# Optimization experiments

Hardware: AMD Instinct MI355X
Metric: run time of the kernel (lower is better)

Reference implementation:

```python
import jax, jax.numpy as jnp
import numpy as np

DIM = 256
CTX_DIM = 256
HEADS = 32
DIM_HEAD = 32
INNER = HEADS * DIM_HEAD


def mish(x):
    return x * jnp.tanh(jax.nn.softplus(x))


def setup_inputs() -> dict:
    key = jax.random.key(0)
    ks = jax.random.split(key, 16)
    B, Lq, Lp = 16, 128, 512
    s = 0.02
    return {
        "x": jax.random.normal(ks[0], (B * Lq, DIM), jnp.float32),
        "context": jax.random.normal(ks[1], (B * Lp, CTX_DIM), jnp.float32),
        "batch_dis": jax.random.normal(ks[2], (B, Lp, Lq, 3), jnp.float32),
        "batch_dis_emb": jax.random.normal(ks[3], (B, Lp, Lq, HEADS), jnp.float32),
        "protein_len": Lp,
        "ligand_len": Lq,
        # params ([in, out] layout, torch Linear transposed)
        "W_qk": jax.random.normal(ks[4], (DIM, INNER), jnp.float32) * s,
        "W_v": jax.random.normal(ks[5], (DIM, INNER), jnp.float32) * s,
        "W_cqk": jax.random.normal(ks[6], (CTX_DIM, INNER), jnp.float32) * s,
        "W_cv": jax.random.normal(ks[7], (CTX_DIM, INNER), jnp.float32) * s,
        "W_m1": jax.random.normal(ks[8], (2 * HEADS, 4 * HEADS), jnp.float32) * s,
        "W_m2": jax.random.normal(ks[9], (4 * HEADS, 2 * HEADS), jnp.float32) * s,
        "b_m2": jnp.zeros((2 * HEADS,), jnp.float32),
        "W_o": jax.random.normal(ks[10], (INNER, DIM), jnp.float32) * s,
        "b_o": jnp.zeros((DIM,), jnp.float32),
        "W_d1": jax.random.normal(ks[11], (HEADS, 2 * HEADS), jnp.float32) * s,
        "b_d1": jnp.zeros((2 * HEADS,), jnp.float32),
        "W_d2": jax.random.normal(ks[12], (2 * HEADS, HEADS), jnp.float32) * s,
        "b_d2": jnp.zeros((HEADS,), jnp.float32),
    }


def reference(x, context, batch_dis, batch_dis_emb, protein_len, ligand_len,
              W_qk, W_v, W_cqk, W_cv, W_m1, W_m2, b_m2, W_o, b_o,
              W_d1, b_d1, W_d2, b_d2):
    h, dh = HEADS, DIM_HEAD
    scale = dh ** -0.5
    B = x.shape[0] // ligand_len
    # projections; split heads: [B, L, h, dh]
    qk = (x @ W_qk).reshape(B, ligand_len, h, dh)
    cqk = (context @ W_cqk).reshape(B, protein_len, h, dh)
    cv = (context @ W_cv).reshape(B, protein_len, h, dh)
    # ligand->protein attention scores: [B, h, Lq, Lp]
    sim = jnp.einsum('bihd,bjhd->bhij', qk, cqk) * scale
    # distance-embedding channels: [B, Lp, Lq, h] -> [B, h, Lq, Lp]
    dis = jnp.transpose(batch_dis_emb, (0, 3, 2, 1))
    s = jnp.concatenate([sim, dis], axis=1)           # [B, 2h, Lq, Lp]
    s = jnp.moveaxis(s, 1, -1)                        # [B, Lq, Lp, 2h]
    s = mish(s @ W_m1) @ W_m2 + b_m2                  # attn_mlp over channel dim
    attn = jax.nn.softmax(s, axis=2)                  # softmax over protein (j)
    # first h heads attend into context values
    out = jnp.einsum('bijh,bjhd->bihd', attn[..., :h], cv)
    out = out.reshape(B * ligand_len, h * dh) @ W_o + b_o   # [N_lig, dim]
    # last h heads aggregate 3D distance vectors
    out_dis = jnp.einsum('bijh,bjid->bidh', attn[..., h:], batch_dis)
    out_dis = out_dis.reshape(B * ligand_len, 3, h)
    out_dis = mish(out_dis @ W_d1 + b_d1) @ W_d2 + b_d2      # [N_lig, 3, h]
    return out, out_dis
```

## Files before the change

### kernel.cpp

```cpp
#include <hip/hip_runtime.h>

typedef unsigned short u16;
typedef unsigned int   u32;
typedef __attribute__((ext_vector_type(8))) short bf16x8;
typedef __attribute__((ext_vector_type(4))) float f32x4;

#define MFMA_BF16 __builtin_amdgcn_mfma_f32_16x16x32_bf16
#define LOG2E 1.4426950408889634f

__device__ __forceinline__ u16 f2bf(float f) {
    u32 x = __builtin_bit_cast(u32, f);
    u32 r = (x + 0x7fffu + ((x >> 16) & 1u)) >> 16;
    return (u16)r;
}
__device__ __forceinline__ u32 cvt_pk_bf16(float lo, float hi) {
    u32 r;
    asm("v_cvt_pk_bf16_f32 %0, %1, %2" : "=v"(r) : "v"(lo), "v"(hi));
    return r;
}
__device__ __forceinline__ float exp2_asm(float x) {
    float r;
    asm("v_exp_f32 %0, %1" : "=v"(r) : "v"(x));
    return r;
}
__device__ __forceinline__ float rcp_asm(float x) {
    float r;
    asm("v_rcp_f32 %0, %1" : "=v"(r) : "v"(x));
    return r;
}
__device__ __forceinline__ float mishf(float x) {
    float e = exp2_asm(x * LOG2E);
    float p = 1.f + e;
    float d = __builtin_fmaf(p, p, 1.f);
    float r = __builtin_fmaf(-2.f, rcp_asm(d), 1.f);
    return x * r;
}

__global__ __launch_bounds__(256) void gemm_mfma(
    const float* __restrict__ A, const float* __restrict__ W, u16* __restrict__ C,
    int M, int N, int K, float scale)
{
    __shared__ u16 As[128 * 40];
    __shared__ u16 Bf[4 * 64 * 8];

    const int tid = threadIdx.x;
    const int lane = tid & 63, wv = tid >> 6;
    const int qd = lane >> 4, ln = lane & 15;
    const int m0 = blockIdx.y * 128, n0 = blockIdx.x * 64;

    f32x4 acc[2][4];
#pragma unroll
    for (int a = 0; a < 2; ++a)
#pragma unroll
        for (int nt = 0; nt < 4; ++nt) acc[a][nt] = (f32x4){0.f, 0.f, 0.f, 0.f};

    for (int k0 = 0; k0 < K; k0 += 32) {
        {
            int r = tid >> 1, kh = (tid & 1) * 16;
            const float* ap = A + (size_t)(m0 + r) * K + k0 + kh;
            float4 a0 = ((const float4*)ap)[0];
            float4 a1 = ((const float4*)ap)[1];
            float4 a2 = ((const float4*)ap)[2];
            float4 a3 = ((const float4*)ap)[3];
            uint4 p0, p1;
            p0.x = cvt_pk_bf16(a0.x, a0.y);
            p0.y = cvt_pk_bf16(a0.z, a0.w);
            p0.z = cvt_pk_bf16(a1.x, a1.y);
            p0.w = cvt_pk_bf16(a1.z, a1.w);
            p1.x = cvt_pk_bf16(a2.x, a2.y);
            p1.y = cvt_pk_bf16(a2.z, a2.w);
            p1.z = cvt_pk_bf16(a3.x, a3.y);
            p1.w = cvt_pk_bf16(a3.z, a3.w);
            *(uint4*)&As[r * 40 + kh]     = p0;
            *(uint4*)&As[r * 40 + kh + 8] = p1;
        }
        {
            int nt = tid >> 6, q = (tid >> 4) & 3, nn = tid & 15;
            const float* wp = W + (size_t)(k0 + q * 8) * N + n0 + nt * 16 + nn;
            float w0 = wp[0], w1 = wp[(size_t)1 * N], w2 = wp[(size_t)2 * N], w3 = wp[(size_t)3 * N];
            float w4 = wp[(size_t)4 * N], w5 = wp[(size_t)5 * N], w6 = wp[(size_t)6 * N], w7 = wp[(size_t)7 * N];
            uint4 u;
            u.x = cvt_pk_bf16(w0, w1);
            u.y = cvt_pk_bf16(w2, w3);
            u.z = cvt_pk_bf16(w4, w5);
            u.w = cvt_pk_bf16(w6, w7);
            *(uint4*)&Bf[tid * 8] = u;
        }
        __syncthreads();
        bf16x8 af0 = *(const bf16x8*)&As[(wv * 32 + ln) * 40 + qd * 8];
        bf16x8 af1 = *(const bf16x8*)&As[(wv * 32 + 16 + ln) * 40 + qd * 8];
#pragma unroll
        for (int nt = 0; nt < 4; ++nt) {
            bf16x8 bfr = *(const bf16x8*)&Bf[(nt * 64 + lane) * 8];
            acc[0][nt] = MFMA_BF16(af0, bfr, acc[0][nt], 0, 0, 0);
            acc[1][nt] = MFMA_BF16(af1, bfr, acc[1][nt], 0, 0, 0);
        }
        __syncthreads();
    }
#pragma unroll
    for (int a = 0; a < 2; ++a)
#pragma unroll
        for (int nt = 0; nt < 4; ++nt) {
            u32 pk0 = cvt_pk_bf16(acc[a][nt][0] * scale, acc[a][nt][1] * scale);
            u32 pk1 = cvt_pk_bf16(acc[a][nt][2] * scale, acc[a][nt][3] * scale);
            size_t base = (size_t)(m0 + wv * 32 + a * 16 + qd * 4) * N + n0 + nt * 16 + ln;
            C[base]               = (u16)pk0;
            C[base + (size_t)N]   = (u16)(pk0 >> 16);
            C[base + (size_t)2*N] = (u16)pk1;
            C[base + (size_t)3*N] = (u16)(pk1 >> 16);
        }
}

__global__ __launch_bounds__(256) void transpose_cv(
    const u16* __restrict__ cv, u16* __restrict__ cvT)
{
    __shared__ u16 T[64 * 80];
    const int tid = threadIdx.x;
    const int ct = blockIdx.x * 64, jt = blockIdx.y * 64, b = blockIdx.z;
    {
        int j_l = tid >> 2, seg = tid & 3;
        const u16* src = cv + (size_t)(b * 512 + jt + j_l) * 1024 + ct + seg * 16;
        uint4 v0 = ((const uint4*)src)[0];
        uint4 v1 = ((const uint4*)src)[1];
        u16* tp = &T[seg * 16 * 80 + j_l];
        tp[0*80] = (u16)(v0.x & 0xffff); tp[1*80] = (u16)(v0.x >> 16);
        tp[2*80] = (u16)(v0.y & 0xffff); tp[3*80] = (u16)(v0.y >> 16);
        tp[4*80] = (u16)(v0.z & 0xffff); tp[5*80] = (u16)(v0.z >> 16);
        tp[6*80] = (u16)(v0.w & 0xffff); tp[7*80] = (u16)(v0.w >> 16);
        tp[8*80] = (u16)(v1.x & 0xffff); tp[9*80] = (u16)(v1.x >> 16);
        tp[10*80] = (u16)(v1.y & 0xffff); tp[11*80] = (u16)(v1.y >> 16);
        tp[12*80] = (u16)(v1.z & 0xffff); tp[13*80] = (u16)(v1.z >> 16);
        tp[14*80] = (u16)(v1.w & 0xffff); tp[15*80] = (u16)(v1.w >> 16);
    }
    __syncthreads();
    {
        int ch_l = tid >> 2, sg = tid & 3;
        u16* dst = cvT + (size_t)(b * 1024 + ct + ch_l) * 512 + jt + sg * 16;
        ((uint4*)dst)[0] = *(const uint4*)&T[ch_l * 80 + sg * 16];
        ((uint4*)dst)[1] = *(const uint4*)&T[ch_l * 80 + sg * 16 + 8];
    }
}

__global__ __launch_bounds__(256) void prep(
    const float* __restrict__ Wo, const float* __restrict__ W1, const float* __restrict__ W2,
    u16* __restrict__ WoT, u16* __restrict__ w1b, u16* __restrict__ w2b)
{
    const int bb = blockIdx.x, t = threadIdx.x;
    if (bb < 256) {
#pragma unroll
        for (int kk = 0; kk < 4; ++kk)
            WoT[(size_t)t * 1024 + bb * 4 + kk] = f2bf(Wo[(size_t)(bb * 4 + kk) * 256 + t]);
    } else {
        for (int u = 0; u < 32; ++u) {
            int idx = t + 256 * u;
            int j = idx & 7, lane = (idx >> 3) & 63, f = idx >> 9;
            int n = lane & 15, q = lane >> 4, ntc = f & 7, ks = f >> 3;
            w1b[idx] = f2bf(W1[(ks * 32 + q * 8 + j) * 128 + ntc * 16 + n]);
        }
        for (int u = 0; u < 32; ++u) {
            int idx = t + 256 * u;
            int j = idx & 7, lane = (idx >> 3) & 63, f = idx >> 9;
            int n = lane & 15, q = lane >> 4, ot = f & 3, ks = f >> 2;
            int k = q * 8 + j;
            int ch = ((k & 1) << 4) | (k >> 1);
            w2b[idx] = f2bf(W2[(ks * 32 + ch) * 64 + ot * 16 + n] * LOG2E);
        }
    }
}

__global__ __launch_bounds__(256, 1) void attn5(
    const u16* __restrict__ qk,
    const u16* __restrict__ cqk,
    const u16* __restrict__ cvT,
    const float* __restrict__ bde,
    const float* __restrict__ bdis,
    const u16* __restrict__ w1b, const u16* __restrict__ w2b,
    const float* __restrict__ b2,
    float* __restrict__ partial)
{
    __shared__ __align__(16) char smem[62976];
    u16*   ES  = (u16*)smem;
    u16*   MT  = (u16*)(smem + 20480);
    float* BD  = (float*)(smem + 25600);
    u16*   EST = (u16*)(smem + 29696);
    u16*   W1B = (u16*)(smem + 54784);

    const int tid = threadIdx.x;
    const int lane = tid & 63, wv = tid >> 6;
    const int qd = lane >> 4, ln = lane & 15;
    const int nblk = blockIdx.x;
    const int xcd = nblk & 7, g = nblk >> 3;
    const int b = xcd * 2 + (g & 1);
    const int r2 = g >> 1;
    const int it = r2 >> 2, jq = r2 & 3;
    const int i0 = it * 16;
    const int pidx = (b * 8 + it) * 4 + jq;

    for (int k = tid; k < 4096; k += 256) ((u32*)W1B)[k] = ((const u32*)w1b)[k];

    float b2r[4];
#pragma unroll
    for (int ot = 0; ot < 4; ++ot) b2r[ot] = b2[ot * 16 + ln] * LOG2E;

    bf16x8 qkf[8];
#pragma unroll
    for (int hh = 0; hh < 8; ++hh) {
        int h = wv * 8 + hh;
        qkf[hh] = *(const bf16x8*)(qk + ((size_t)(b * 128 + i0 + ln)) * 1024 + h * 32 + qd * 8);
    }

    f32x4 oacc[8][2];
#pragma unroll
    for (int a = 0; a < 8; ++a)
#pragma unroll
        for (int c = 0; c < 2; ++c) oacc[a][c] = (f32x4){0.f, 0.f, 0.f, 0.f};
    float dn[4][4] = {};
    float dd[4][3][2] = {};

    __syncthreads();

#pragma clang loop unroll(disable)
    for (int ps = 0; ps < 8; ++ps) {
        const int jg0 = jq * 128 + ps * 16;

        {
            const u16* crow = cqk + (size_t)(b * 512 + jg0 + ln) * 1024 + qd * 8;
#pragma unroll
            for (int hh = 0; hh < 4; ++hh) {
                const int h0 = wv * 8 + hh * 2;
                bf16x8 b0 = *(const bf16x8*)(crow + h0 * 32);
                bf16x8 b1 = *(const bf16x8*)(crow + (h0 + 1) * 32);
                f32x4 c0 = (f32x4){0.f, 0.f, 0.f, 0.f}, c1 = c0;
                c0 = MFMA_BF16(qkf[hh * 2],     b0, c0, 0, 0, 0);
                c1 = MFMA_BF16(qkf[hh * 2 + 1], b1, c1, 0, 0, 0);
#pragma unroll
                for (int r = 0; r < 4; ++r)
                    *(u32*)&ES[((qd * 4 + r) * 16 + ln) * 40 + h0] = cvt_pk_bf16(c0[r], c1[r]);
            }
        }
        {
            int ii = tid & 15, jj = tid >> 4;
            const float* sp = bdis + ((size_t)(b * 512 + jg0 + jj) * 128 + i0 + ii) * 3;
            float4 v4;
            v4.x = sp[0]; v4.y = sp[1]; v4.z = sp[2]; v4.w = 0.f;
            *(float4*)&BD[(ii * 16 + jj) * 4] = v4;
        }
        __syncthreads();

#pragma unroll
        for (int s = 0; s < 4; ++s) {
            const int i_loc = wv * 4 + s;
            bf16x8 af0 = *(const bf16x8*)&ES[(i_loc * 16 + ln) * 40 + qd * 8];
            bf16x8 af1;
            {
                const float* dp = bde + (((size_t)(b * 512 + jg0 + ln)) * 128 + i0 + i_loc) * 32 + qd * 8;
                float4 a0 = ((const float4*)dp)[0];
                float4 a1 = ((const float4*)dp)[1];
                uint4 u;
                u.x = cvt_pk_bf16(a0.x, a0.y);
                u.y = cvt_pk_bf16(a0.z, a0.w);
                u.z = cvt_pk_bf16(a1.x, a1.y);
                u.w = cvt_pk_bf16(a1.z, a1.w);
                af1 = __builtin_bit_cast(bf16x8, u);
            }
            f32x4 uacc[4];
#pragma unroll
            for (int ot = 0; ot < 4; ++ot) uacc[ot] = (f32x4){0.f, 0.f, 0.f, 0.f};
            u16* mt = MT + wv * 640;
#pragma unroll
            for (int cg = 0; cg < 4; ++cg) {
                bf16x8 w00 = *(const bf16x8*)&W1B[((cg * 2 + 0) * 64 + lane) * 8];
                bf16x8 w01 = *(const bf16x8*)&W1B[((cg * 2 + 1) * 64 + lane) * 8];
                bf16x8 w10 = *(const bf16x8*)&W1B[((8 + cg * 2 + 0) * 64 + lane) * 8];
                bf16x8 w11 = *(const bf16x8*)&W1B[((8 + cg * 2 + 1) * 64 + lane) * 8];
                f32x4 t0 = (f32x4){0.f, 0.f, 0.f, 0.f}, t1 = t0;
                t0 = MFMA_BF16(af0, w00, t0, 0, 0, 0);
                t0 = MFMA_BF16(af1, w10, t0, 0, 0, 0);
                t1 = MFMA_BF16(af0, w01, t1, 0, 0, 0);
                t1 = MFMA_BF16(af1, w11, t1, 0, 0, 0);
#pragma unroll
                for (int r = 0; r < 4; ++r) {
                    u32 pk = cvt_pk_bf16(mishf(t0[r]), mishf(t1[r]));
                    *(u32*)&mt[(qd * 4 + r) * 40 + (ln << 1)] = pk;
                }
                bf16x8 ta = *(const bf16x8*)&mt[ln * 40 + qd * 8];
#pragma unroll
                for (int ot = 0; ot < 4; ++ot) {
                    bf16x8 wf = *(const bf16x8*)(w2b + ((size_t)(cg * 4 + ot) * 64 + lane) * 8);
                    uacc[ot] = MFMA_BF16(ta, wf, uacc[ot], 0, 0, 0);
                }
            }
            float Ev[4][4];
#pragma unroll
            for (int ot = 0; ot < 4; ++ot) {
#pragma unroll
                for (int r = 0; r < 4; ++r) Ev[ot][r] = exp2_asm(uacc[ot][r] + b2r[ot]);
                dn[s][ot] += (Ev[ot][0] + Ev[ot][1]) + (Ev[ot][2] + Ev[ot][3]);
            }
#pragma unroll
            for (int r = 0; r < 4; ++r) {
                float4 bp = *(const float4*)&BD[(i_loc * 16 + qd * 4 + r) * 4];
                dd[s][0][0] += Ev[2][r] * bp.x; dd[s][0][1] += Ev[3][r] * bp.x;
                dd[s][1][0] += Ev[2][r] * bp.y; dd[s][1][1] += Ev[3][r] * bp.y;
                dd[s][2][0] += Ev[2][r] * bp.z; dd[s][2][1] += Ev[3][r] * bp.z;
            }
#pragma unroll
            for (int ot = 0; ot < 2; ++ot) {
                const int base = (ot * 16 + ln) * 392 + i_loc * 24 + qd * 4;
                *(u32*)&EST[base]     = cvt_pk_bf16(Ev[ot][0], Ev[ot][1]);
                *(u32*)&EST[base + 2] = cvt_pk_bf16(Ev[ot][2], Ev[ot][3]);
            }
        }
        __syncthreads();

#pragma unroll
        for (int hh = 0; hh < 8; ++hh) {
            const int h = wv * 8 + hh;
            bf16x8 af = (bf16x8){0, 0, 0, 0, 0, 0, 0, 0};
            if (qd < 2) af = *(const bf16x8*)&EST[h * 392 + ln * 24 + qd * 8];
#pragma unroll
            for (int nt = 0; nt < 2; ++nt) {
                bf16x8 bfr = (bf16x8){0, 0, 0, 0, 0, 0, 0, 0};
                if (qd < 2)
                    bfr = *(const bf16x8*)(cvT + ((size_t)(b * 1024 + h * 32 + nt * 16 + ln)) * 512 + jg0 + qd * 8);
                oacc[hh][nt] = MFMA_BF16(af, bfr, oacc[hh][nt], 0, 0, 0);
            }
        }
        __syncthreads();
    }

    float* P = partial + (size_t)pidx * 18944;
#pragma unroll
    for (int hh = 0; hh < 8; ++hh)
#pragma unroll
        for (int nt = 0; nt < 2; ++nt)
#pragma unroll
            for (int r = 0; r < 4; ++r)
                P[(size_t)(qd * 4 + r) * 1024 + (wv * 8 + hh) * 32 + nt * 16 + ln] = oacc[hh][nt][r];
#pragma unroll
    for (int s = 0; s < 4; ++s)
#pragma unroll
        for (int ot = 0; ot < 4; ++ot) {
            float v = dn[s][ot];
            v += __shfl_xor(v, 16, 64);
            v += __shfl_xor(v, 32, 64);
            if (qd == 0) P[16384 + (wv * 4 + s) * 64 + ot * 16 + ln] = v;
        }
#pragma unroll
    for (int s = 0; s < 4; ++s)
#pragma unroll
        for (int d = 0; d < 3; ++d)
#pragma unroll
            for (int o = 0; o < 2; ++o) {
                float v = dd[s][d][o];
                v += __shfl_xor(v, 16, 64);
                v += __shfl_xor(v, 32, 64);
                if (qd == 0) P[17408 + (wv * 4 + s) * 96 + d * 32 + o * 16 + ln] = v;
            }
}

__global__ __launch_bounds__(256, 2) void finalize(
    const float* __restrict__ partial, const u16* __restrict__ WoT,
    const float* __restrict__ bo,
    const float* __restrict__ Wd1, const float* __restrict__ bd1,
    const float* __restrict__ Wd2, const float* __restrict__ bd2,
    float* __restrict__ out0, float* __restrict__ out1)
{
    __shared__ float denomL[1024];
    __shared__ u16 preL[16 * 1032];
    __shared__ float odisL[1536];
    __shared__ float r1L[3072];

    const int tid = threadIdx.x;
    const int f = blockIdx.x;
    const int b = f >> 3, it = f & 7;
    const int row0 = b * 128 + it * 16;
    const float* P0 = partial + (size_t)(f * 4 + 0) * 18944;
    const float* P1 = partial + (size_t)(f * 4 + 1) * 18944;
    const float* P2 = partial + (size_t)(f * 4 + 2) * 18944;
    const float* P3 = partial + (size_t)(f * 4 + 3) * 18944;

    for (int k = tid; k < 1024; k += 256)
        denomL[k] = P0[16384 + k] + P1[16384 + k] + P2[16384 + k] + P3[16384 + k];
    __syncthreads();

    {
        const int h = tid >> 3;
#pragma unroll
        for (int i = 0; i < 16; ++i) {
            float4 a = *(const float4*)&P0[(size_t)i * 1024 + tid * 4];
            float4 bq = *(const float4*)&P1[(size_t)i * 1024 + tid * 4];
            float4 c = *(const float4*)&P2[(size_t)i * 1024 + tid * 4];
            float4 d = *(const float4*)&P3[(size_t)i * 1024 + tid * 4];
            float rdn = 1.f / denomL[i * 64 + h];
            u32 p0 = cvt_pk_bf16((a.x + bq.x + c.x + d.x) * rdn, (a.y + bq.y + c.y + d.y) * rdn);
            u32 p1 = cvt_pk_bf16((a.z + bq.z + c.z + d.z) * rdn, (a.w + bq.w + c.w + d.w) * rdn);
            *(uint2*)(void*)&preL[i * 1032 + tid * 4] = make_uint2(p0, p1);
        }
    }
    for (int idx = tid; idx < 1536; idx += 256) {
        int i = idx / 96, rm = idx % 96, h = rm & 31;
        odisL[idx] = (P0[17408 + idx] + P1[17408 + idx] + P2[17408 + idx] + P3[17408 + idx])
                     / denomL[i * 64 + 32 + h];
    }
    __syncthreads();

    {
        const int lane = tid & 63, wv = tid >> 6;
        const int qd = lane >> 4, ln = lane & 15;
        f32x4 acc[4];
#pragma unroll
        for (int nt = 0; nt < 4; ++nt) acc[nt] = (f32x4){0.f, 0.f, 0.f, 0.f};
#pragma clang loop unroll(disable)
        for (int ks = 0; ks < 32; ++ks) {
            bf16x8 af = *(const bf16x8*)&preL[ln * 1032 + ks * 32 + qd * 8];
#pragma unroll
            for (int nt = 0; nt < 4; ++nt) {
                bf16x8 wf = *(const bf16x8*)(WoT + ((size_t)(wv * 64 + nt * 16 + ln)) * 1024 + ks * 32 + qd * 8);
                acc[nt] = MFMA_BF16(af, wf, acc[nt], 0, 0, 0);
            }
        }
#pragma unroll
        for (int nt = 0; nt < 4; ++nt) {
            int col = wv * 64 + nt * 16 + ln;
            float bv = bo[col];
#pragma unroll
            for (int r = 0; r < 4; ++r)
                out0[(size_t)(row0 + qd * 4 + r) * 256 + col] = acc[nt][r] + bv;
        }
    }

    for (int idx = tid; idx < 3072; idx += 256) {
        int i = idx / 192, rm = idx % 192, d = rm / 64, c = rm & 63;
        float t = bd1[c];
#pragma unroll
        for (int hh = 0; hh < 32; ++hh)
            t += odisL[i * 96 + d * 32 + hh] * Wd1[hh * 64 + c];
        r1L[idx] = mishf(t);
    }
    __syncthreads();
    for (int idx = tid; idx < 1536; idx += 256) {
        int i = idx / 96, rm = idx % 96, d = rm >> 5, h = rm & 31;
        float v = bd2[h];
#pragma unroll
        for (int c = 0; c < 64; ++c)
            v += r1L[i * 192 + d * 64 + c] * Wd2[c * 32 + h];
        out1[(size_t)(row0 + i) * 96 + d * 32 + h] = v;
    }
}

extern "C" void kernel_launch(void* const* d_in, const int* in_sizes, int n_in,
                              void* d_out, int out_size, void* d_ws, size_t ws_size,
                              hipStream_t stream) {
    const float* x    = (const float*)d_in[0];
    const float* ctx  = (const float*)d_in[1];
    const float* bdis = (const float*)d_in[2];
    const float* bde  = (const float*)d_in[3];
    const float* Wqk  = (const float*)d_in[6];
    const float* Wcqk = (const float*)d_in[8];
    const float* Wcv  = (const float*)d_in[9];
    const float* Wm1  = (const float*)d_in[10];
    const float* Wm2  = (const float*)d_in[11];
    const float* bm2  = (const float*)d_in[12];
    const float* Wo   = (const float*)d_in[13];
    const float* bo   = (const float*)d_in[14];
    const float* Wd1  = (const float*)d_in[15];
    const float* bd1  = (const float*)d_in[16];
    const float* Wd2  = (const float*)d_in[17];
    const float* bd2  = (const float*)d_in[18];

    char* ws = (char*)d_ws;
    u16* qk_ws  = (u16*)(ws);
    u16* cqk_ws = (u16*)(ws + 4194304);
    u16* cvT_ws = (u16*)(ws + 20971520);
    u16* w1b    = (u16*)(ws + 37748736);
    u16* w2b    = (u16*)(ws + 37765120);
    u16* WoT    = (u16*)(ws + 37781504);
    float* part = (float*)(ws + 38305792);
    u16* cv_rm  = (u16*)(ws + 38305792);

    float* out0 = (float*)d_out;
    float* out1 = out0 + (size_t)2048 * 256;

    const float SCALE = 0.17677669529663687f;

    prep<<<257, 256, 0, stream>>>(Wo, Wm1, Wm2, WoT, w1b, w2b);
    gemm_mfma<<<dim3(16, 16), 256, 0, stream>>>(x,   Wqk,  qk_ws,  2048, 1024, 256, SCALE);
    gemm_mfma<<<dim3(16, 64), 256, 0, stream>>>(ctx, Wcqk, cqk_ws, 8192, 1024, 256, 1.0f);
    gemm_mfma<<<dim3(16, 64), 256, 0, stream>>>(ctx, Wcv,  cv_rm,  8192, 1024, 256, 1.0f);
    transpose_cv<<<dim3(16, 8, 16), 256, 0, stream>>>(cv_rm, cvT_ws);
    attn5<<<512, 256, 0, stream>>>(qk_ws, cqk_ws, cvT_ws, bde, bdis, w1b, w2b, bm2, part);
    finalize<<<128, 256, 0, stream>>>(part, WoT, bo, Wd1, bd1, Wd2, bd2, out0, out1);
}
```

Before: 577.3 us.

## Register-prefetch next tile's cqk, bde and bdis loads across loop iterations

Software-pipelines the main protein-tile loop by loading the next iteration's cqk fragments, bde embedding values and bdis distances into registers while the current tile's MLP runs. The BD shared buffer is written from those prefetched registers after the MLP stage. The per-wave MT scratch is also double-buffered by cg parity, which removes a read-after-write dependence between consecutive chunks, and shared memory grows to fit the second buffer. The goal is to hide global-memory latency behind compute, at the cost of more registers, which could cause spills at launch_bounds(256,1).

```diff
diff --git a/kernel.cpp b/kernel.cpp
--- a/kernel.cpp
+++ b/kernel.cpp
@@ -178,12 +178,12 @@
     const float* __restrict__ b2,
     float* __restrict__ partial)
 {
-    __shared__ __align__(16) char smem[62976];
+    __shared__ __align__(16) char smem[68096];
     u16*   ES  = (u16*)smem;
     u16*   MT  = (u16*)(smem + 20480);
-    float* BD  = (float*)(smem + 25600);
-    u16*   EST = (u16*)(smem + 29696);
-    u16*   W1B = (u16*)(smem + 54784);
+    float* BD  = (float*)(smem + 30720);
+    u16*   EST = (u16*)(smem + 34816);
+    u16*   W1B = (u16*)(smem + 59904);
 
     const int tid = threadIdx.x;
     const int lane = tid & 63, wv = tid >> 6;
@@ -209,6 +209,28 @@
         qkf[hh] = *(const bf16x8*)(qk + ((size_t)(b * 128 + i0 + ln)) * 1024 + h * 32 + qd * 8);
     }
 
+    const int ii = tid & 15, jj = tid >> 4;
+
+    bf16x8 cqk_pf[8];
+    float4 bde_pf[8];
+    float bdp0, bdp1, bdp2;
+    {
+        const u16* crow = cqk + (size_t)(b * 512 + jq * 128 + ln) * 1024 + qd * 8;
+#pragma unroll
+        for (int hh = 0; hh < 8; ++hh)
+            cqk_pf[hh] = *(const bf16x8*)(crow + (wv * 8 + hh) * 32);
+#pragma unroll
+        for (int s2 = 0; s2 < 4; ++s2) {
+            const float* dps = bde + (((size_t)(b * 512 + jq * 128 + ln)) * 128 + i0 + wv * 4 + s2) * 32 + qd * 8;
+            bde_pf[s2 * 2]     = ((const float4*)dps)[0];
+            bde_pf[s2 * 2 + 1] = ((const float4*)dps)[1];
+        }
+        const float* sp = bdis + ((size_t)(b * 512 + jq * 128 + jj) * 128 + i0 + ii) * 3;
+        bdp0 = sp[0]; bdp1 = sp[1]; bdp2 = sp[2];
+        float* dp2 = &BD[(ii * 16 + jj) * 4];
+        dp2[0] = bdp0; dp2[1] = bdp1; dp2[2] = bdp2;
+    }
+
     f32x4 oacc[8][2];
 #pragma unroll
     for (int a = 0; a < 8; ++a)
@@ -224,28 +246,41 @@
         const int jg0 = jq * 128 + ps * 16;
 
         {
-            const u16* crow = cqk + (size_t)(b * 512 + jg0 + ln) * 1024 + qd * 8;
+            bf16x8 cqk_use[8];
+#pragma unroll
+            for (int hh = 0; hh < 8; ++hh) cqk_use[hh] = cqk_pf[hh];
 #pragma unroll
             for (int hh = 0; hh < 4; ++hh) {
                 const int h0 = wv * 8 + hh * 2;
-                bf16x8 b0 = *(const bf16x8*)(crow + h0 * 32);
-                bf16x8 b1 = *(const bf16x8*)(crow + (h0 + 1) * 32);
                 f32x4 c0 = (f32x4){0.f, 0.f, 0.f, 0.f}, c1 = c0;
-                c0 = MFMA_BF16(qkf[hh * 2],     b0, c0, 0, 0, 0);
-                c1 = MFMA_BF16(qkf[hh * 2 + 1], b1, c1, 0, 0, 0);
+                c0 = MFMA_BF16(qkf[hh * 2],     cqk_use[hh * 2],     c0, 0, 0, 0);
+                c1 = MFMA_BF16(qkf[hh * 2 + 1], cqk_use[hh * 2 + 1], c1, 0, 0, 0);
 #pragma unroll
                 for (int r = 0; r < 4; ++r)
                     *(u32*)&ES[((qd * 4 + r) * 16 + ln) * 40 + h0] = cvt_pk_bf16(c0[r], c1[r]);
             }
         }
+        __syncthreads();
+
+        const int psn = (ps < 7) ? ps + 1 : 7;
+        const int jgn = jq * 128 + psn * 16;
+        float4 bde_use[8];
+#pragma unroll
+        for (int k = 0; k < 8; ++k) bde_use[k] = bde_pf[k];
         {
-            int ii = tid & 15, jj = tid >> 4;
-            const float* sp = bdis + ((size_t)(b * 512 + jg0 + jj) * 128 + i0 + ii) * 3;
-            float4 v4;
-            v4.x = sp[0]; v4.y = sp[1]; v4.z = sp[2]; v4.w = 0.f;
-            *(float4*)&BD[(ii * 16 + jj) * 4] = v4;
-        }
-        __syncthreads();
+            const u16* crow = cqk + (size_t)(b * 512 + jgn + ln) * 1024 + qd * 8;
+#pragma unroll
+            for (int hh = 0; hh < 8; ++hh)
+                cqk_pf[hh] = *(const bf16x8*)(crow + (wv * 8 + hh) * 32);
+#pragma unroll
+            for (int s2 = 0; s2 < 4; ++s2) {
+                const float* dps = bde + (((size_t)(b * 512 + jgn + ln)) * 128 + i0 + wv * 4 + s2) * 32 + qd * 8;
+                bde_pf[s2 * 2]     = ((const float4*)dps)[0];
+                bde_pf[s2 * 2 + 1] = ((const float4*)dps)[1];
+            }
+            const float* sp = bdis + ((size_t)(b * 512 + jgn + jj) * 128 + i0 + ii) * 3;
+            bdp0 = sp[0]; bdp1 = sp[1]; bdp2 = sp[2];
+        }
 
 #pragma unroll
         for (int s = 0; s < 4; ++s) {
@@ -253,9 +288,8 @@
             bf16x8 af0 = *(const bf16x8*)&ES[(i_loc * 16 + ln) * 40 + qd * 8];
             bf16x8 af1;
             {
-                const float* dp = bde + (((size_t)(b * 512 + jg0 + ln)) * 128 + i0 + i_loc) * 32 + qd * 8;
-                float4 a0 = ((const float4*)dp)[0];
-                float4 a1 = ((const float4*)dp)[1];
+                float4 a0 = bde_use[s * 2];
+                float4 a1 = bde_use[s * 2 + 1];
                 uint4 u;
                 u.x = cvt_pk_bf16(a0.x, a0.y);
                 u.y = cvt_pk_bf16(a0.z, a0.w);
@@ -266,9 +300,9 @@
             f32x4 uacc[4];
 #pragma unroll
             for (int ot = 0; ot < 4; ++ot) uacc[ot] = (f32x4){0.f, 0.f, 0.f, 0.f};
-            u16* mt = MT + wv * 640;
 #pragma unroll
             for (int cg = 0; cg < 4; ++cg) {
+                u16* mtp = MT + wv * 1280 + (cg & 1) * 640;
                 bf16x8 w00 = *(const bf16x8*)&W1B[((cg * 2 + 0) * 64 + lane) * 8];
                 bf16x8 w01 = *(const bf16x8*)&W1B[((cg * 2 + 1) * 64 + lane) * 8];
                 bf16x8 w10 = *(const bf16x8*)&W1B[((8 + cg * 2 + 0) * 64 + lane) * 8];
@@ -281,9 +315,9 @@
 #pragma unroll
                 for (int r = 0; r < 4; ++r) {
                     u32 pk = cvt_pk_bf16(mishf(t0[r]), mishf(t1[r]));
-                    *(u32*)&mt[(qd * 4 + r) * 40 + (ln << 1)] = pk;
+                    *(u32*)&mtp[(qd * 4 + r) * 40 + (ln << 1)] = pk;
                 }
-                bf16x8 ta = *(const bf16x8*)&mt[ln * 40 + qd * 8];
+                bf16x8 ta = *(const bf16x8*)&mtp[ln * 40 + qd * 8];
 #pragma unroll
                 for (int ot = 0; ot < 4; ++ot) {
                     bf16x8 wf = *(const bf16x8*)(w2b + ((size_t)(cg * 4 + ot) * 64 + lane) * 8);
@@ -313,6 +347,10 @@
         }
         __syncthreads();
 
+        {
+            float* dp2 = &BD[(ii * 16 + jj) * 4];
+            dp2[0] = bdp0; dp2[1] = bdp1; dp2[2] = bdp2;
+        }
 #pragma unroll
         for (int hh = 0; hh < 8; ++hh) {
             const int h = wv * 8 + hh;
```

New measurement: 537.7 us. -6.8%, faster.
